# Optimization experiments

Measured on AMD Instinct MI355X. Metric: run time of the kernel, lower is better.

## Reference

```python
import jax, jax.numpy as jnp
import numpy as np
from functools import partial

SOM_SHAPE = (100, 100)
INPUT_SIZE = 256
BATCH = 1024
INIT_LR = 0.5
INIT_RADIUS = max(SOM_SHAPE) / 2.0  # 50.0


def setup_inputs() -> dict:
    key = jax.random.key(0)
    k1, k2 = jax.random.split(key)
    x = jax.random.normal(k1, (BATCH, INPUT_SIZE), dtype=jnp.float32)
    weights = jax.random.normal(k2, (*SOM_SHAPE, INPUT_SIZE), dtype=jnp.float32) * 0.1
    return {"x": x, "weights": weights, "epoch": 10, "total_epochs": 100}


def reference(x, weights, epoch, total_epochs):
    H, W = SOM_SHAPE
    decay = 1.0 - epoch / total_epochs
    lr = jnp.float32(INIT_LR * decay)
    radius = jnp.float32(INIT_RADIUS * decay)

    # --- get_bmu: squared euclidean distances x (B,D) vs weights (H*W,D) ---
    wf = weights.reshape(-1, INPUT_SIZE)                       # (HW, D)
    d2 = (jnp.sum(x * x, axis=1, keepdims=True)                # (B, 1)
          - 2.0 * (x @ wf.T)                                   # (B, HW)
          + jnp.sum(wf * wf, axis=1))                          # (HW,)
    bmu_idx = jnp.argmin(d2, axis=1)                           # (B,)
    by = (bmu_idx // W).astype(jnp.float32)                    # (B,)
    bx = (bmu_idx % W).astype(jnp.float32)

    # --- get_neighborhood: gaussian over grid distance to BMU ---
    yy = jnp.arange(H, dtype=jnp.float32)[:, None]             # (H, 1)
    xx = jnp.arange(W, dtype=jnp.float32)[None, :]             # (1, W)
    grid_d2 = ((by[:, None, None] - yy) ** 2
               + (bx[:, None, None] - xx) ** 2)                # (B, H, W)
    neigh = jnp.exp(-grid_d2 / (2.0 * radius ** 2))            # (B, H, W)

    # --- update_weights: sequential per-sample EMA update (recurrence) ---
    def step(w, inp):
        xi, ni = inp  # (D,), (H, W)
        w = w + lr * ni[..., None] * (xi[None, None, :] - w)
        return w, None

    new_weights, _ = jax.lax.scan(step, weights, (x, neigh))
    return new_weights
```

## Files before the change

kernel.cpp:

```cpp
#include <hip/hip_runtime.h>
#include <hip/hip_fp16.h>

typedef unsigned long long ull;
typedef unsigned short ushort_t;
typedef unsigned int u32;
typedef short bf16x8 __attribute__((ext_vector_type(8)));
typedef _Float16 f16x8 __attribute__((ext_vector_type(8)));
typedef float f32x4 __attribute__((ext_vector_type(4)));

#define NC 10000
#define D_ 256
#define B_ 1024
#define W_ 100
#define LD 10240
#define FIXMARGIN 0.06f
#define SHORTCAP 128

__device__ __forceinline__ void gl_lds16(const void* g, void* l) {
    __builtin_amdgcn_global_load_lds(
        (const __attribute__((address_space(1))) u32*)g,
        (__attribute__((address_space(3))) u32*)l,
        16, 0, 0);
}

__device__ __forceinline__ int xcd_swz(int orig, int nwg) {
    int q = nwg >> 3, r = nwg & 7;
    int xcd = orig & 7, off = orig >> 3;
    return (xcd < r ? xcd * (q + 1) : r * (q + 1) + (xcd - r) * q) + off;
}

__device__ __forceinline__ unsigned fkey(float f) {
    unsigned u = __float_as_uint(f);
    return (u & 0x80000000u) ? ~u : (u | 0x80000000u);
}
__device__ __forceinline__ float unfkey(unsigned k) {
    unsigned u = (k & 0x80000000u) ? (k ^ 0x80000000u) : ~k;
    return __uint_as_float(u);
}

__device__ __forceinline__ ushort_t f2bf(float f) {
    unsigned u = __float_as_uint(f);
    unsigned r = (u + 0x7fffu + ((u >> 16) & 1u)) >> 16;
    return (ushort_t)r;
}

__device__ __forceinline__ void decay_params(const int* ep, const int* tp, float& lr, float& inv2r2) {
    double decay = 1.0 - (double)(*ep) / (double)(*tp);
    lr = (float)(0.5 * decay);
    float radius = (float)(50.0 * decay);
    inv2r2 = 1.0f / (2.0f * radius * radius);
}

__global__ void k_init(ull* pk1, float* wnorm) {
    int i = blockIdx.x * 256 + threadIdx.x;
    if (i < B_) pk1[i] = ~0ull;
    else if (i < B_ + 128) wnorm[NC + (i - B_)] = __builtin_inff();
}

__global__ __launch_bounds__(256) void k_split_w(const float* __restrict__ w, __half* __restrict__ wh,
                                                 float* __restrict__ wnorm) {
    int cell = blockIdx.x * 4 + (threadIdx.x >> 6);
    int lane = threadIdx.x & 63;
    float4 v = *reinterpret_cast<const float4*>(&w[(size_t)cell * D_ + lane * 4]);
    float s = v.x * v.x + v.y * v.y + v.z * v.z + v.w * v.w;
    __half hb[4];
    float e[4] = {v.x, v.y, v.z, v.w};
    #pragma unroll
    for (int i = 0; i < 4; ++i) hb[i] = __float2half(e[i]);
    *reinterpret_cast<uint2*>(&wh[(size_t)cell * D_ + lane * 4]) = *reinterpret_cast<uint2*>(hb);
    #pragma unroll
    for (int off = 32; off; off >>= 1) s += __shfl_xor(s, off);
    if (lane == 0) wnorm[cell] = s;
}

__global__ __launch_bounds__(256) void k_prep_x(const float* __restrict__ x, __half* __restrict__ xh,
                                                ushort_t* __restrict__ xhT) {
    __shared__ ushort_t tile[64][65];
    int b0 = blockIdx.x * 64, d0 = blockIdx.y * 64;
    int tid = threadIdx.x;
    #pragma unroll
    for (int r = 0; r < 16; ++r) {
        int idx = r * 256 + tid;
        int i = idx >> 6, j = idx & 63;
        float v = x[(size_t)(b0 + i) * D_ + d0 + j];
        xh[(size_t)(b0 + i) * D_ + d0 + j] = __float2half(v);
        tile[j][i] = f2bf(v);
    }
    __syncthreads();
    #pragma unroll
    for (int r = 0; r < 2; ++r) {
        int f = r * 256 + tid;
        int row = f >> 3, u = f & 7;
        ushort_t v[8];
        #pragma unroll
        for (int e = 0; e < 8; ++e) v[e] = tile[row][u * 8 + e];
        *reinterpret_cast<uint4*>(&xhT[(size_t)(d0 + row) * B_ + b0 + u * 8]) =
            *reinterpret_cast<uint4*>(v);
    }
}

__global__ __launch_bounds__(512) void k_scores_mfma(const __half* __restrict__ wh, const __half* __restrict__ xh,
                                                     const float* __restrict__ wnorm, __half* __restrict__ h,
                                                     ull* __restrict__ pk1) {
    __shared__ __align__(16) __half As[128 * 64];
    __shared__ __align__(16) __half Bs[128 * 64];
    const int tid = threadIdx.x;
    int orig = blockIdx.y * gridDim.x + blockIdx.x;
    int wgid = xcd_swz(orig, 8 * 79);
    const int b0 = (wgid & 7) * 128;
    const int c0 = (wgid >> 3) * 128;
    const int wid = tid >> 6, lane = tid & 63;
    const int wc = wid >> 2;
    const int wb = wid & 3;
    const int g4 = lane >> 4, l16 = lane & 15;

    f32x4 acc[4][2] = {};

    for (int k0 = 0; k0 < D_; k0 += 64) {
        if (k0) __syncthreads();
        #pragma unroll
        for (int r = 0; r < 2; ++r) {
            int f = tid + r * 512;
            int row = f >> 3, u = f & 7;
            int ug = (u ^ (row & 7)) * 8;
            int cc = c0 + row; if (cc > NC - 1) cc = NC - 1;
            gl_lds16(&wh[(size_t)cc * D_ + k0 + ug], &As[(f & ~63) * 8]);
            gl_lds16(&xh[(size_t)(b0 + row) * D_ + k0 + ug], &Bs[(f & ~63) * 8]);
        }
        __syncthreads();
        #pragma unroll
        for (int kh = 0; kh < 2; ++kh) {
            int ubase = kh * 4 + g4;
            f16x8 bfr[2];
            #pragma unroll
            for (int fn = 0; fn < 2; ++fn) {
                int rowb = wb * 32 + fn * 16 + l16;
                bfr[fn] = *reinterpret_cast<const f16x8*>(&Bs[rowb * 64 + ((ubase ^ (rowb & 7)) * 8)]);
            }
            #pragma unroll
            for (int fm = 0; fm < 4; ++fm) {
                int rowa = wc * 64 + fm * 16 + l16;
                f16x8 af = *reinterpret_cast<const f16x8*>(&As[rowa * 64 + ((ubase ^ (rowa & 7)) * 8)]);
                #pragma unroll
                for (int fn = 0; fn < 2; ++fn)
                    acc[fm][fn] = __builtin_amdgcn_mfma_f32_16x16x32_f16(af, bfr[fn], acc[fm][fn], 0, 0, 0);
            }
        }
    }

    #pragma unroll
    for (int fm = 0; fm < 4; ++fm) {
        int cb = c0 + wc * 64 + fm * 16 + g4 * 4;
        #pragma unroll
        for (int fn = 0; fn < 2; ++fn) {
            int b = b0 + wb * 32 + fn * 16 + l16;
            __half hv[4];
            #pragma unroll
            for (int r = 0; r < 4; ++r) hv[r] = __float2half(acc[fm][fn][r]);
            *reinterpret_cast<uint2*>(&h[(size_t)b * LD + cb]) = *reinterpret_cast<uint2*>(hv);
        }
    }

    ull best[2] = {~0ull, ~0ull};
    #pragma unroll
    for (int fm = 0; fm < 4; ++fm) {
        int cb = c0 + wc * 64 + fm * 16 + g4 * 4;
        float4 wn4 = *reinterpret_cast<const float4*>(&wnorm[cb]);
        float wna[4] = {wn4.x, wn4.y, wn4.z, wn4.w};
        #pragma unroll
        for (int fn = 0; fn < 2; ++fn)
            #pragma unroll
            for (int r = 0; r < 4; ++r) {
                float s = wna[r] - 2.0f * acc[fm][fn][r];
                ull p = ((ull)fkey(s) << 32) | (unsigned)(cb + r);
                if (p < best[fn]) best[fn] = p;
            }
    }
    #pragma unroll
    for (int fn = 0; fn < 2; ++fn) {
        ull o = __shfl_xor(best[fn], 16); best[fn] = o < best[fn] ? o : best[fn];
        o = __shfl_xor(best[fn], 32);     best[fn] = o < best[fn] ? o : best[fn];
    }
    if (g4 == 0) {
        atomicMin(&pk1[b0 + wb * 32 + l16], best[0]);
        atomicMin(&pk1[b0 + wb * 32 + 16 + l16], best[1]);
    }
}

__global__ __launch_bounds__(256) void k_fix(const __half* __restrict__ h, const float* __restrict__ wnorm,
                                             const float* __restrict__ x, const float* __restrict__ w,
                                             const ull* __restrict__ pk1, int2* __restrict__ bxy) {
    __shared__ int cnt;
    __shared__ int cand[SHORTCAP];
    __shared__ ull sbest[4];
    int b = blockIdx.x, tid = threadIdx.x;
    if (tid == 0) cnt = 0;
    __syncthreads();
    float thr = unfkey((unsigned)(pk1[b] >> 32)) + FIXMARGIN;
    for (int ch = 0; ch < 10; ++ch) {
        int c = ch * 1024 + tid * 4;
        if (c < NC) {
            __half hv[4];
            *reinterpret_cast<uint2*>(hv) = *reinterpret_cast<const uint2*>(&h[(size_t)b * LD + c]);
            float4 wn = *reinterpret_cast<const float4*>(&wnorm[c]);
            float we[4] = {wn.x, wn.y, wn.z, wn.w};
            #pragma unroll
            for (int e = 0; e < 4; ++e) {
                float s = we[e] - 2.0f * (float)hv[e];
                if (s <= thr) {
                    int p = atomicAdd(&cnt, 1);
                    if (p < SHORTCAP) cand[p] = c + e;
                }
            }
        }
    }
    __syncthreads();
    int n = cnt;
    int wid = tid >> 6, lane = tid & 63;
    float4 xv = *reinterpret_cast<const float4*>(&x[(size_t)b * D_ + lane * 4]);
    ull best = ~0ull;
    if (n <= SHORTCAP) {
        for (int i = wid; i < n; i += 4) {
            int c = cand[i];
            float4 wv = *reinterpret_cast<const float4*>(&w[(size_t)c * D_ + lane * 4]);
            float p = wv.x * (wv.x - 2.0f * xv.x) + wv.y * (wv.y - 2.0f * xv.y)
                    + wv.z * (wv.z - 2.0f * xv.z) + wv.w * (wv.w - 2.0f * xv.w);
            #pragma unroll
            for (int off = 32; off; off >>= 1) p += __shfl_xor(p, off);
            if (lane == 0) {
                ull pk = ((ull)fkey(p) << 32) | (unsigned)c;
                best = pk < best ? pk : best;
            }
        }
    } else {
        for (int c = wid; c < NC; c += 4) {
            float4 wv = *reinterpret_cast<const float4*>(&w[(size_t)c * D_ + lane * 4]);
            float p = wv.x * (wv.x - 2.0f * xv.x) + wv.y * (wv.y - 2.0f * xv.y)
                    + wv.z * (wv.z - 2.0f * xv.z) + wv.w * (wv.w - 2.0f * xv.w);
            #pragma unroll
            for (int off = 32; off; off >>= 1) p += __shfl_xor(p, off);
            if (lane == 0) {
                ull pk = ((ull)fkey(p) << 32) | (unsigned)c;
                best = pk < best ? pk : best;
            }
        }
    }
    if (lane == 0) sbest[wid] = best;
    __syncthreads();
    if (tid == 0) {
        ull bb = sbest[0];
        #pragma unroll
        for (int k = 1; k < 4; ++k) bb = sbest[k] < bb ? sbest[k] : bb;
        int c = (int)(unsigned)(bb & 0xffffffffull);
        bxy[b] = make_int2(c / W_, c % W_);
    }
}

__global__ __launch_bounds__(256) void k_scan(const int2* __restrict__ bxy, const int* __restrict__ ep,
                                              const int* __restrict__ tp, ushort_t* __restrict__ coefT,
                                              float* __restrict__ T) {
    __shared__ float E[W_];
    float lr, inv2r2;
    decay_params(ep, tp, lr, inv2r2);
    if (threadIdx.x < W_) {
        float d = (float)threadIdx.x;
        E[threadIdx.x] = __expf(-d * d * inv2r2);
    }
    __syncthreads();

    int g = blockIdx.x * 256 + threadIdx.x;
    int c = g >> 3, t = g & 7;
    if (c >= NC) return;
    int cy = c / W_, cx = c % W_;
    int base = t * 128;

    float P = 1.0f;
    for (int i = base; i < base + 128; ++i) {
        int2 p = bxy[i];
        int dy = abs(p.x - cy), dx = abs(p.y - cx);
        float a = lr * E[dy] * E[dx];
        P *= (1.0f - a);
    }
    int gbase = (threadIdx.x & 63) & ~7;
    float M = 1.0f;
    #pragma unroll
    for (int k = 1; k < 8; ++k) {
        float pk = __shfl(P, gbase + k, 64);
        if (k > t) M *= pk;
    }
    if (t == 0) T[c] = M * P;

    float s = M;
    for (int seg = 15; seg >= 0; --seg) {
        ushort_t buf[8];
        #pragma unroll
        for (int e = 7; e >= 0; --e) {
            int i = base + seg * 8 + e;
            int2 p = bxy[i];
            int dy = abs(p.x - cy), dx = abs(p.y - cx);
            float a = lr * E[dy] * E[dx];
            buf[e] = f2bf(a * s);
            s *= (1.0f - a);
        }
        *reinterpret_cast<uint4*>(&coefT[(size_t)c * B_ + base + seg * 8]) =
            *reinterpret_cast<uint4*>(buf);
    }
}

__global__ __launch_bounds__(256) void k_update(const ushort_t* __restrict__ coefT, const ushort_t* __restrict__ xhT,
                                                const float* __restrict__ T, const float* __restrict__ w0,
                                                float* __restrict__ out) {
    __shared__ __align__(16) ushort_t As[64 * 64];
    __shared__ __align__(16) ushort_t Bs[64 * 64];
    const int tid = threadIdx.x;
    int orig = blockIdx.y * gridDim.x + blockIdx.x;
    int wgid = xcd_swz(orig, 4 * 157);
    const int d0 = (wgid & 3) * 64;
    const int c0 = (wgid >> 2) * 64;
    const int wid = tid >> 6, lane = tid & 63;
    const int wc = wid >> 1, wd = wid & 1;
    const int g4 = lane >> 4, l16 = lane & 15;

    f32x4 acc[2][2] = {};

    for (int k0 = 0; k0 < B_; k0 += 64) {
        if (k0) __syncthreads();
        #pragma unroll
        for (int r = 0; r < 2; ++r) {
            int f = tid + r * 256;
            int row = f >> 3, u = f & 7;
            int ug = (u ^ (row & 7)) * 8;
            int cc = c0 + row; if (cc > NC - 1) cc = NC - 1;
            gl_lds16(&coefT[(size_t)cc * B_ + k0 + ug], &As[(f & ~63) * 8]);
            gl_lds16(&xhT[(size_t)(d0 + row) * B_ + k0 + ug], &Bs[(f & ~63) * 8]);
        }
        __syncthreads();
        #pragma unroll
        for (int kh = 0; kh < 2; ++kh) {
            bf16x8 af[2], bfr[2];
            int ubase = kh * 4 + g4;
            #pragma unroll
            for (int fm = 0; fm < 2; ++fm) {
                int rowa = wc * 32 + fm * 16 + l16;
                af[fm] = *reinterpret_cast<const bf16x8*>(&As[rowa * 64 + ((ubase ^ (rowa & 7)) * 8)]);
                int rowb = wd * 32 + fm * 16 + l16;
                bfr[fm] = *reinterpret_cast<const bf16x8*>(&Bs[rowb * 64 + ((ubase ^ (rowb & 7)) * 8)]);
            }
            #pragma unroll
            for (int fm = 0; fm < 2; ++fm)
                #pragma unroll
                for (int fn = 0; fn < 2; ++fn)
                    acc[fm][fn] = __builtin_amdgcn_mfma_f32_16x16x32_bf16(af[fm], bfr[fn], acc[fm][fn], 0, 0, 0);
        }
    }

    #pragma unroll
    for (int fm = 0; fm < 2; ++fm) {
        #pragma unroll
        for (int r = 0; r < 4; ++r) {
            int c = c0 + wc * 32 + fm * 16 + g4 * 4 + r;
            if (c < NC) {
                float t = T[c];
                #pragma unroll
                for (int fn = 0; fn < 2; ++fn) {
                    int d = d0 + wd * 32 + fn * 16 + l16;
                    out[(size_t)c * D_ + d] = fmaf(t, w0[(size_t)c * D_ + d], acc[fm][fn][r]);
                }
            }
        }
    }
}

__global__ void k_initfix(ull* packed_fix) {
    int i = blockIdx.x * 256 + threadIdx.x;
    if (i < B_) packed_fix[i] = ~0ull;
}
__global__ __launch_bounds__(256) void k_exact_bmu(const float* __restrict__ x, const float* __restrict__ w,
                                                   ull* __restrict__ packed_fix) {
    int b = blockIdx.x;
    int wid = threadIdx.x >> 6, lane = threadIdx.x & 63;
    float4 xv = *reinterpret_cast<const float4*>(&x[(size_t)b * D_ + lane * 4]);
    ull best = ~0ull;
    for (int c = wid; c < NC; c += 4) {
        float4 wv = *reinterpret_cast<const float4*>(&w[(size_t)c * D_ + lane * 4]);
        float p = wv.x * (wv.x - 2.0f * xv.x) + wv.y * (wv.y - 2.0f * xv.y)
                + wv.z * (wv.z - 2.0f * xv.z) + wv.w * (wv.w - 2.0f * xv.w);
        #pragma unroll
        for (int off = 32; off; off >>= 1) p += __shfl_xor(p, off);
        if (lane == 0) {
            ull pk = ((ull)fkey(p) << 32) | (unsigned)c;
            best = pk < best ? pk : best;
        }
    }
    if (lane == 0) atomicMin(&packed_fix[b], best);
}
__global__ void k_decode_force(const ull* __restrict__ packed_fix, float2* __restrict__ xy) {
    int i = blockIdx.x * 256 + threadIdx.x;
    if (i < B_) {
        int c = (int)(unsigned)(packed_fix[i] & 0xffffffffull);
        xy[i] = make_float2((float)(c / W_), (float)(c % W_));
    }
}
__global__ __launch_bounds__(256) void k_update_fallback(const float* __restrict__ x, const float* __restrict__ w0,
                                                         const float2* __restrict__ xy, const int* ep, const int* tp,
                                                         float* __restrict__ out) {
    int c = blockIdx.x;
    int d = threadIdx.x;
    float cyf = (float)(c / W_), cxf = (float)(c % W_);
    float lr, inv2r2;
    decay_params(ep, tp, lr, inv2r2);
    float acc = w0[(size_t)c * D_ + d];
    for (int i = 0; i < B_; ++i) {
        float2 p = xy[i];
        float dy = p.x - cyf, dx = p.y - cxf;
        float a = lr * __expf(-(dy * dy + dx * dx) * inv2r2);
        acc = fmaf(a, x[(size_t)i * D_ + d] - acc, acc);
    }
    out[(size_t)c * D_ + d] = acc;
}

extern "C" void kernel_launch(void* const* d_in, const int* in_sizes, int n_in,
                              void* d_out, int out_size, void* d_ws, size_t ws_size,
                              hipStream_t stream) {
    const float* x = (const float*)d_in[0];
    const float* w = (const float*)d_in[1];
    const int* ep = (const int*)d_in[2];
    const int* tp = (const int*)d_in[3];
    float* out = (float*)d_out;

    char* ws = (char*)d_ws;
    ull* pk1        = (ull*)ws;
    int2* bxy       = (int2*)(ws + 16384);
    float2* xyf     = (float2*)(ws + 16384);
    float* T        = (float*)(ws + 24576);
    float* wnorm    = (float*)(ws + 65536);
    ushort_t* xhT   = (ushort_t*)(ws + 131072);
    __half* xh      = (__half*)(ws + 655360);
    __half* wh      = (__half*)(ws + 1179648);
    ushort_t* coefT = (ushort_t*)(ws + 6553600);
    __half* h       = (__half*)(ws + 27262976);
    size_t required = 27262976 + (size_t)B_ * LD * 2;

    if (ws_size >= required) {
        k_init<<<5, 256, 0, stream>>>(pk1, wnorm);
        k_split_w<<<NC / 4, 256, 0, stream>>>(w, wh, wnorm);
        k_prep_x<<<dim3(B_ / 64, D_ / 64), 256, 0, stream>>>(x, xh, xhT);
        k_scores_mfma<<<dim3(B_ / 128, (NC + 127) / 128), 512, 0, stream>>>(wh, xh, wnorm, h, pk1);
        k_fix<<<B_, 256, 0, stream>>>(h, wnorm, x, w, pk1, bxy);
        k_scan<<<(NC * 8 + 255) / 256, 256, 0, stream>>>(bxy, ep, tp, coefT, T);
        k_update<<<dim3(D_ / 64, (NC + 63) / 64), 256, 0, stream>>>(coefT, xhT, T, w, out);
    } else {
        k_initfix<<<4, 256, 0, stream>>>(pk1);
        k_exact_bmu<<<B_, 256, 0, stream>>>(x, w, pk1);
        k_decode_force<<<4, 256, 0, stream>>>(pk1, xyf);
        k_update_fallback<<<NC, 256, 0, stream>>>(x, w, xyf, ep, tp, out);
    }
}
```

Baseline: 92.22 us.

## Replace fp16 score matrix with per-tile top-2 candidates and double-buffer GEMM staging

```diff
diff --git a/kernel.cpp b/kernel.cpp
--- a/kernel.cpp
+++ b/kernel.cpp
@@ -12,9 +12,9 @@
 #define D_ 256
 #define B_ 1024
 #define W_ 100
-#define LD 10240
-#define FIXMARGIN 0.06f
-#define SHORTCAP 128
+#define NT 79
+#define PKS 160
+#define TAU 0.10f
 
 __device__ __forceinline__ void gl_lds16(const void* g, void* l) {
     __builtin_amdgcn_global_load_lds(
@@ -51,64 +51,68 @@
     inv2r2 = 1.0f / (2.0f * radius * radius);
 }
 
-__global__ void k_init(ull* pk1, float* wnorm) {
-    int i = blockIdx.x * 256 + threadIdx.x;
-    if (i < B_) pk1[i] = ~0ull;
-    else if (i < B_ + 128) wnorm[NC + (i - B_)] = __builtin_inff();
-}
-
-__global__ __launch_bounds__(256) void k_split_w(const float* __restrict__ w, __half* __restrict__ wh,
-                                                 float* __restrict__ wnorm) {
-    int cell = blockIdx.x * 4 + (threadIdx.x >> 6);
-    int lane = threadIdx.x & 63;
-    float4 v = *reinterpret_cast<const float4*>(&w[(size_t)cell * D_ + lane * 4]);
-    float s = v.x * v.x + v.y * v.y + v.z * v.z + v.w * v.w;
-    __half hb[4];
-    float e[4] = {v.x, v.y, v.z, v.w};
-    #pragma unroll
-    for (int i = 0; i < 4; ++i) hb[i] = __float2half(e[i]);
-    *reinterpret_cast<uint2*>(&wh[(size_t)cell * D_ + lane * 4]) = *reinterpret_cast<uint2*>(hb);
-    #pragma unroll
-    for (int off = 32; off; off >>= 1) s += __shfl_xor(s, off);
-    if (lane == 0) wnorm[cell] = s;
-}
-
-__global__ __launch_bounds__(256) void k_prep_x(const float* __restrict__ x, __half* __restrict__ xh,
-                                                ushort_t* __restrict__ xhT) {
-    __shared__ ushort_t tile[64][65];
-    int b0 = blockIdx.x * 64, d0 = blockIdx.y * 64;
+__device__ __forceinline__ void merge2(ull& a1, ull& a2, ull c1, ull c2) {
+    ull m1 = a1 < c1 ? a1 : c1;
+    ull hi = a1 < c1 ? c1 : a1;
+    ull lo2 = a2 < c2 ? a2 : c2;
+    a2 = hi < lo2 ? hi : lo2;
+    a1 = m1;
+}
+
+__global__ __launch_bounds__(256) void k_prep(const float* __restrict__ w, const float* __restrict__ x,
+                                              __half* __restrict__ wh, float* __restrict__ wnorm,
+                                              __half* __restrict__ xh, ushort_t* __restrict__ xhT) {
+    int bid = blockIdx.x;
     int tid = threadIdx.x;
-    #pragma unroll
-    for (int r = 0; r < 16; ++r) {
-        int idx = r * 256 + tid;
-        int i = idx >> 6, j = idx & 63;
-        float v = x[(size_t)(b0 + i) * D_ + d0 + j];
-        xh[(size_t)(b0 + i) * D_ + d0 + j] = __float2half(v);
-        tile[j][i] = f2bf(v);
-    }
-    __syncthreads();
-    #pragma unroll
-    for (int r = 0; r < 2; ++r) {
-        int f = r * 256 + tid;
-        int row = f >> 3, u = f & 7;
-        ushort_t v[8];
-        #pragma unroll
-        for (int e = 0; e < 8; ++e) v[e] = tile[row][u * 8 + e];
-        *reinterpret_cast<uint4*>(&xhT[(size_t)(d0 + row) * B_ + b0 + u * 8]) =
-            *reinterpret_cast<uint4*>(v);
+    if (bid < NC / 4) {
+        int cell = bid * 4 + (tid >> 6);
+        int lane = tid & 63;
+        float4 v = *reinterpret_cast<const float4*>(&w[(size_t)cell * D_ + lane * 4]);
+        float s = v.x * v.x + v.y * v.y + v.z * v.z + v.w * v.w;
+        __half hb[4];
+        float e[4] = {v.x, v.y, v.z, v.w};
+        #pragma unroll
+        for (int i = 0; i < 4; ++i) hb[i] = __float2half(e[i]);
+        *reinterpret_cast<uint2*>(&wh[(size_t)cell * D_ + lane * 4]) = *reinterpret_cast<uint2*>(hb);
+        #pragma unroll
+        for (int off = 32; off; off >>= 1) s += __shfl_xor(s, off);
+        if (lane == 0) wnorm[cell] = s;
+    } else {
+        __shared__ ushort_t tile[64][65];
+        int idx = bid - NC / 4;
+        int b0 = (idx & 15) * 64, d0 = (idx >> 4) * 64;
+        #pragma unroll
+        for (int r = 0; r < 16; ++r) {
+            int f = r * 256 + tid;
+            int i = f >> 6, j = f & 63;
+            float v = x[(size_t)(b0 + i) * D_ + d0 + j];
+            xh[(size_t)(b0 + i) * D_ + d0 + j] = __float2half(v);
+            tile[j][i] = f2bf(v);
+        }
+        __syncthreads();
+        #pragma unroll
+        for (int r = 0; r < 2; ++r) {
+            int f = r * 256 + tid;
+            int row = f >> 3, u = f & 7;
+            ushort_t v[8];
+            #pragma unroll
+            for (int e = 0; e < 8; ++e) v[e] = tile[row][u * 8 + e];
+            *reinterpret_cast<uint4*>(&xhT[(size_t)(d0 + row) * B_ + b0 + u * 8]) =
+                *reinterpret_cast<uint4*>(v);
+        }
     }
 }
 
 __global__ __launch_bounds__(512) void k_scores_mfma(const __half* __restrict__ wh, const __half* __restrict__ xh,
-                                                     const float* __restrict__ wnorm, __half* __restrict__ h,
-                                                     ull* __restrict__ pk1) {
-    __shared__ __align__(16) __half As[128 * 64];
-    __shared__ __align__(16) __half Bs[128 * 64];
+                                                     const float* __restrict__ wnorm, ull* __restrict__ pkt) {
+    __shared__ __align__(16) __half As[2][128 * 64];
+    __shared__ __align__(16) __half Bs[2][128 * 64];
     const int tid = threadIdx.x;
     int orig = blockIdx.y * gridDim.x + blockIdx.x;
-    int wgid = xcd_swz(orig, 8 * 79);
+    int wgid = xcd_swz(orig, 8 * NT);
     const int b0 = (wgid & 7) * 128;
     const int c0 = (wgid >> 3) * 128;
+    const int tile = wgid >> 3;
     const int wid = tid >> 6, lane = tid & 63;
     const int wc = wid >> 2;
     const int wb = wid & 3;
@@ -116,18 +120,23 @@
 
     f32x4 acc[4][2] = {};
 
-    for (int k0 = 0; k0 < D_; k0 += 64) {
-        if (k0) __syncthreads();
+    auto STAGE = [&](int buf, int k0) {
         #pragma unroll
         for (int r = 0; r < 2; ++r) {
             int f = tid + r * 512;
             int row = f >> 3, u = f & 7;
             int ug = (u ^ (row & 7)) * 8;
             int cc = c0 + row; if (cc > NC - 1) cc = NC - 1;
-            gl_lds16(&wh[(size_t)cc * D_ + k0 + ug], &As[(f & ~63) * 8]);
-            gl_lds16(&xh[(size_t)(b0 + row) * D_ + k0 + ug], &Bs[(f & ~63) * 8]);
-        }
-        __syncthreads();
+            gl_lds16(&wh[(size_t)cc * D_ + k0 + ug], &As[buf][(f & ~63) * 8]);
+            gl_lds16(&xh[(size_t)(b0 + row) * D_ + k0 + ug], &Bs[buf][(f & ~63) * 8]);
+        }
+    };
+
+    STAGE(0, 0);
+    __syncthreads();
+    for (int kt = 0; kt < 4; ++kt) {
+        int cur = kt & 1;
+        if (kt < 3) STAGE(cur ^ 1, (kt + 1) * 64);
         #pragma unroll
         for (int kh = 0; kh < 2; ++kh) {
             int ubase = kh * 4 + g4;
@@ -135,33 +144,21 @@
             #pragma unroll
             for (int fn = 0; fn < 2; ++fn) {
                 int rowb = wb * 32 + fn * 16 + l16;
-                bfr[fn] = *reinterpret_cast<const f16x8*>(&Bs[rowb * 64 + ((ubase ^ (rowb & 7)) * 8)]);
+                bfr[fn] = *reinterpret_cast<const f16x8*>(&Bs[cur][rowb * 64 + ((ubase ^ (rowb & 7)) * 8)]);
             }
             #pragma unroll
             for (int fm = 0; fm < 4; ++fm) {
                 int rowa = wc * 64 + fm * 16 + l16;
-                f16x8 af = *reinterpret_cast<const f16x8*>(&As[rowa * 64 + ((ubase ^ (rowa & 7)) * 8)]);
+                f16x8 af = *reinterpret_cast<const f16x8*>(&As[cur][rowa * 64 + ((ubase ^ (rowa & 7)) * 8)]);
                 #pragma unroll
                 for (int fn = 0; fn < 2; ++fn)
                     acc[fm][fn] = __builtin_amdgcn_mfma_f32_16x16x32_f16(af, bfr[fn], acc[fm][fn], 0, 0, 0);
             }
         }
-    }
-
-    #pragma unroll
-    for (int fm = 0; fm < 4; ++fm) {
-        int cb = c0 + wc * 64 + fm * 16 + g4 * 4;
-        #pragma unroll
-        for (int fn = 0; fn < 2; ++fn) {
-            int b = b0 + wb * 32 + fn * 16 + l16;
-            __half hv[4];
-            #pragma unroll
-            for (int r = 0; r < 4; ++r) hv[r] = __float2half(acc[fm][fn][r]);
-            *reinterpret_cast<uint2*>(&h[(size_t)b * LD + cb]) = *reinterpret_cast<uint2*>(hv);
-        }
-    }
-
-    ull best[2] = {~0ull, ~0ull};
+        __syncthreads();
+    }
+
+    ull m1[2] = {~0ull, ~0ull}, m2[2] = {~0ull, ~0ull};
     #pragma unroll
     for (int fm = 0; fm < 4; ++fm) {
         int cb = c0 + wc * 64 + fm * 16 + g4 * 4;
@@ -172,86 +169,109 @@
             #pragma unroll
             for (int r = 0; r < 4; ++r) {
                 float s = wna[r] - 2.0f * acc[fm][fn][r];
-                ull p = ((ull)fkey(s) << 32) | (unsigned)(cb + r);
-                if (p < best[fn]) best[fn] = p;
+                ull p = (cb + r < NC) ? (((ull)fkey(s) << 32) | (unsigned)(cb + r)) : ~0ull;
+                merge2(m1[fn], m2[fn], p, ~0ull);
             }
     }
     #pragma unroll
     for (int fn = 0; fn < 2; ++fn) {
-        ull o = __shfl_xor(best[fn], 16); best[fn] = o < best[fn] ? o : best[fn];
-        o = __shfl_xor(best[fn], 32);     best[fn] = o < best[fn] ? o : best[fn];
-    }
+        #pragma unroll
+        for (int off = 16; off <= 32; off <<= 1) {
+            ull o1 = __shfl_xor(m1[fn], off), o2 = __shfl_xor(m2[fn], off);
+            merge2(m1[fn], m2[fn], o1, o2);
+        }
+    }
+    ull* sm1 = (ull*)&As[0][0];
+    ull* sm2 = sm1 + 256;
     if (g4 == 0) {
-        atomicMin(&pk1[b0 + wb * 32 + l16], best[0]);
-        atomicMin(&pk1[b0 + wb * 32 + 16 + l16], best[1]);
-    }
-}
-
-__global__ __launch_bounds__(256) void k_fix(const __half* __restrict__ h, const float* __restrict__ wnorm,
-                                             const float* __restrict__ x, const float* __restrict__ w,
-                                             const ull* __restrict__ pk1, int2* __restrict__ bxy) {
-    __shared__ int cnt;
-    __shared__ int cand[SHORTCAP];
-    __shared__ ull sbest[4];
-    int b = blockIdx.x, tid = threadIdx.x;
-    if (tid == 0) cnt = 0;
-    __syncthreads();
-    float thr = unfkey((unsigned)(pk1[b] >> 32)) + FIXMARGIN;
-    for (int ch = 0; ch < 10; ++ch) {
-        int c = ch * 1024 + tid * 4;
+        #pragma unroll
+        for (int fn = 0; fn < 2; ++fn) {
+            int bl = wb * 32 + fn * 16 + l16;
+            sm1[wc * 128 + bl] = m1[fn];
+            sm2[wc * 128 + bl] = m2[fn];
+        }
+    }
+    __syncthreads();
+    if (tid < 128) {
+        ull a1 = sm1[tid], a2 = sm2[tid];
+        merge2(a1, a2, sm1[128 + tid], sm2[128 + tid]);
+        size_t base = (size_t)(b0 + tid) * PKS + tile * 2;
+        pkt[base] = a1;
+        pkt[base + 1] = a2;
+    }
+}
+
+__global__ __launch_bounds__(128) void k_bmu(const ull* __restrict__ pkt, const float* __restrict__ x,
+                                             const float* __restrict__ w, int2* __restrict__ bxy) {
+    __shared__ ull s1[2], s2[2];
+    __shared__ int candList[NT];
+    __shared__ int candCnt;
+    int b = blockIdx.x;
+    int tid = threadIdx.x, lane = tid & 63, wv = tid >> 6;
+
+    ull a1 = ~0ull, a2 = ~0ull;
+    if (tid < NT) {
+        a1 = pkt[(size_t)b * PKS + tid * 2];
+        a2 = pkt[(size_t)b * PKS + tid * 2 + 1];
+    }
+    #pragma unroll
+    for (int off = 1; off <= 32; off <<= 1) {
+        ull o1 = __shfl_xor(a1, off), o2 = __shfl_xor(a2, off);
+        merge2(a1, a2, o1, o2);
+    }
+    if (lane == 0) { s1[wv] = a1; s2[wv] = a2; }
+    __syncthreads();
+    a1 = s1[0]; a2 = s2[0];
+    merge2(a1, a2, s1[1], s2[1]);
+    float f1 = unfkey((unsigned)(a1 >> 32));
+    float f2 = unfkey((unsigned)(a2 >> 32));
+    if (f2 - f1 >= TAU) {
+        if (tid == 0) {
+            int c = (int)(unsigned)(a1 & 0xffffffffull);
+            bxy[b] = make_int2(c / W_, c % W_);
+        }
+        return;
+    }
+    if (tid == 0) candCnt = 0;
+    __syncthreads();
+    if (tid < NT) {
+        ull mt = pkt[(size_t)b * PKS + tid * 2];
+        if (unfkey((unsigned)(mt >> 32)) <= f1 + TAU) {
+            int p = atomicAdd(&candCnt, 1);
+            candList[p] = tid;
+        }
+    }
+    __syncthreads();
+    int n = candCnt;
+    ull best = ~0ull;
+    const float* xr = &x[(size_t)b * D_];
+    for (int ci = 0; ci < n; ++ci) {
+        int t = candList[ci];
+        int c = t * 128 + tid;
         if (c < NC) {
-            __half hv[4];
-            *reinterpret_cast<uint2*>(hv) = *reinterpret_cast<const uint2*>(&h[(size_t)b * LD + c]);
-            float4 wn = *reinterpret_cast<const float4*>(&wnorm[c]);
-            float we[4] = {wn.x, wn.y, wn.z, wn.w};
-            #pragma unroll
-            for (int e = 0; e < 4; ++e) {
-                float s = we[e] - 2.0f * (float)hv[e];
-                if (s <= thr) {
-                    int p = atomicAdd(&cnt, 1);
-                    if (p < SHORTCAP) cand[p] = c + e;
-                }
-            }
-        }
-    }
-    __syncthreads();
-    int n = cnt;
-    int wid = tid >> 6, lane = tid & 63;
-    float4 xv = *reinterpret_cast<const float4*>(&x[(size_t)b * D_ + lane * 4]);
-    ull best = ~0ull;
-    if (n <= SHORTCAP) {
-        for (int i = wid; i < n; i += 4) {
-            int c = cand[i];
-            float4 wv = *reinterpret_cast<const float4*>(&w[(size_t)c * D_ + lane * 4]);
-            float p = wv.x * (wv.x - 2.0f * xv.x) + wv.y * (wv.y - 2.0f * xv.y)
-                    + wv.z * (wv.z - 2.0f * xv.z) + wv.w * (wv.w - 2.0f * xv.w);
-            #pragma unroll
-            for (int off = 32; off; off >>= 1) p += __shfl_xor(p, off);
-            if (lane == 0) {
-                ull pk = ((ull)fkey(p) << 32) | (unsigned)c;
-                best = pk < best ? pk : best;
-            }
-        }
-    } else {
-        for (int c = wid; c < NC; c += 4) {
-            float4 wv = *reinterpret_cast<const float4*>(&w[(size_t)c * D_ + lane * 4]);
-            float p = wv.x * (wv.x - 2.0f * xv.x) + wv.y * (wv.y - 2.0f * xv.y)
-                    + wv.z * (wv.z - 2.0f * xv.z) + wv.w * (wv.w - 2.0f * xv.w);
-            #pragma unroll
-            for (int off = 32; off; off >>= 1) p += __shfl_xor(p, off);
-            if (lane == 0) {
-                ull pk = ((ull)fkey(p) << 32) | (unsigned)c;
-                best = pk < best ? pk : best;
-            }
-        }
-    }
-    if (lane == 0) sbest[wid] = best;
+            const float* wr = &w[(size_t)c * D_];
+            float p = 0.f;
+            #pragma unroll
+            for (int d = 0; d < D_; d += 4) {
+                float4 wv4 = *reinterpret_cast<const float4*>(&wr[d]);
+                float4 xv4 = *reinterpret_cast<const float4*>(&xr[d]);
+                p += wv4.x * (wv4.x - 2.0f * xv4.x) + wv4.y * (wv4.y - 2.0f * xv4.y)
+                   + wv4.z * (wv4.z - 2.0f * xv4.z) + wv4.w * (wv4.w - 2.0f * xv4.w);
+            }
+            ull pk = ((ull)fkey(p) << 32) | (unsigned)c;
+            best = pk < best ? pk : best;
+        }
+    }
+    #pragma unroll
+    for (int off = 1; off <= 32; off <<= 1) {
+        ull o = __shfl_xor(best, off);
+        best = o < best ? o : best;
+    }
+    if (lane == 0) s1[wv] = best;
     __syncthreads();
     if (tid == 0) {
-        ull bb = sbest[0];
-        #pragma unroll
-        for (int k = 1; k < 4; ++k) bb = sbest[k] < bb ? sbest[k] : bb;
-        int c = (int)(unsigned)(bb & 0xffffffffull);
+        best = s1[0] < s1[1] ? s1[0] : s1[1];
+        int c = (int)(unsigned)(best & 0xffffffffull);
         bxy[b] = make_int2(c / W_, c % W_);
     }
 }
@@ -310,8 +330,8 @@
 __global__ __launch_bounds__(256) void k_update(const ushort_t* __restrict__ coefT, const ushort_t* __restrict__ xhT,
                                                 const float* __restrict__ T, const float* __restrict__ w0,
                                                 float* __restrict__ out) {
-    __shared__ __align__(16) ushort_t As[64 * 64];
-    __shared__ __align__(16) ushort_t Bs[64 * 64];
+    __shared__ __align__(16) ushort_t As[2][64 * 64];
+    __shared__ __align__(16) ushort_t Bs[2][64 * 64];
     const int tid = threadIdx.x;
     int orig = blockIdx.y * gridDim.x + blockIdx.x;
     int wgid = xcd_swz(orig, 4 * 157);
@@ -323,18 +343,23 @@
 
     f32x4 acc[2][2] = {};
 
-    for (int k0 = 0; k0 < B_; k0 += 64) {
-        if (k0) __syncthreads();
+    auto STAGE = [&](int buf, int k0) {
         #pragma unroll
         for (int r = 0; r < 2; ++r) {
             int f = tid + r * 256;
             int row = f >> 3, u = f & 7;
             int ug = (u ^ (row & 7)) * 8;
             int cc = c0 + row; if (cc > NC - 1) cc = NC - 1;
-            gl_lds16(&coefT[(size_t)cc * B_ + k0 + ug], &As[(f & ~63) * 8]);
-            gl_lds16(&xhT[(size_t)(d0 + row) * B_ + k0 + ug], &Bs[(f & ~63) * 8]);
-        }
-        __syncthreads();
+            gl_lds16(&coefT[(size_t)cc * B_ + k0 + ug], &As[buf][(f & ~63) * 8]);
+            gl_lds16(&xhT[(size_t)(d0 + row) * B_ + k0 + ug], &Bs[buf][(f & ~63) * 8]);
+        }
+    };
+
+    STAGE(0, 0);
+    __syncthreads();
+    for (int kt = 0; kt < 16; ++kt) {
+        int cur = kt & 1;
+        if (kt < 15) STAGE(cur ^ 1, (kt + 1) * 64);
         #pragma unroll
         for (int kh = 0; kh < 2; ++kh) {
             bf16x8 af[2], bfr[2];
@@ -342,9 +367,9 @@
             #pragma unroll
             for (int fm = 0; fm < 2; ++fm) {
                 int rowa = wc * 32 + fm * 16 + l16;
-                af[fm] = *reinterpret_cast<const bf16x8*>(&As[rowa * 64 + ((ubase ^ (rowa & 7)) * 8)]);
+                af[fm] = *reinterpret_cast<const bf16x8*>(&As[cur][rowa * 64 + ((ubase ^ (rowa & 7)) * 8)]);
                 int rowb = wd * 32 + fm * 16 + l16;
-                bfr[fm] = *reinterpret_cast<const bf16x8*>(&Bs[rowb * 64 + ((ubase ^ (rowb & 7)) * 8)]);
+                bfr[fm] = *reinterpret_cast<const bf16x8*>(&Bs[cur][rowb * 64 + ((ubase ^ (rowb & 7)) * 8)]);
             }
             #pragma unroll
             for (int fm = 0; fm < 2; ++fm)
@@ -352,6 +377,7 @@
                 for (int fn = 0; fn < 2; ++fn)
                     acc[fm][fn] = __builtin_amdgcn_mfma_f32_16x16x32_bf16(af[fm], bfr[fn], acc[fm][fn], 0, 0, 0);
         }
+        __syncthreads();
     }
 
     #pragma unroll
@@ -429,7 +455,7 @@
     float* out = (float*)d_out;
 
     char* ws = (char*)d_ws;
-    ull* pk1        = (ull*)ws;
+    ull* packed_fix = (ull*)(ws + 8192);
     int2* bxy       = (int2*)(ws + 16384);
     float2* xyf     = (float2*)(ws + 16384);
     float* T        = (float*)(ws + 24576);
@@ -438,21 +464,19 @@
     __half* xh      = (__half*)(ws + 655360);
     __half* wh      = (__half*)(ws + 1179648);
     ushort_t* coefT = (ushort_t*)(ws + 6553600);
-    __half* h       = (__half*)(ws + 27262976);
-    size_t required = 27262976 + (size_t)B_ * LD * 2;
+    ull* pkt        = (ull*)(ws + 27262976);
+    size_t required = 27262976 + (size_t)B_ * PKS * 8;
 
     if (ws_size >= required) {
-        k_init<<<5, 256, 0, stream>>>(pk1, wnorm);
-        k_split_w<<<NC / 4, 256, 0, stream>>>(w, wh, wnorm);
-        k_prep_x<<<dim3(B_ / 64, D_ / 64), 256, 0, stream>>>(x, xh, xhT);
-        k_scores_mfma<<<dim3(B_ / 128, (NC + 127) / 128), 512, 0, stream>>>(wh, xh, wnorm, h, pk1);
-        k_fix<<<B_, 256, 0, stream>>>(h, wnorm, x, w, pk1, bxy);
+        k_prep<<<NC / 4 + 64, 256, 0, stream>>>(w, x, wh, wnorm, xh, xhT);
+        k_scores_mfma<<<dim3(8, NT), 512, 0, stream>>>(wh, xh, wnorm, pkt);
+        k_bmu<<<B_, 128, 0, stream>>>(pkt, x, w, bxy);
         k_scan<<<(NC * 8 + 255) / 256, 256, 0, stream>>>(bxy, ep, tp, coefT, T);
-        k_update<<<dim3(D_ / 64, (NC + 63) / 64), 256, 0, stream>>>(coefT, xhT, T, w, out);
+        k_update<<<dim3(4, 157), 256, 0, stream>>>(coefT, xhT, T, w, out);
     } else {
-        k_initfix<<<4, 256, 0, stream>>>(pk1);
-        k_exact_bmu<<<B_, 256, 0, stream>>>(x, w, pk1);
-        k_decode_force<<<4, 256, 0, stream>>>(pk1, xyf);
+        k_initfix<<<4, 256, 0, stream>>>(packed_fix);
+        k_exact_bmu<<<B_, 256, 0, stream>>>(x, w, packed_fix);
+        k_decode_force<<<4, 256, 0, stream>>>(packed_fix, xyf);
         k_update_fallback<<<NC, 256, 0, stream>>>(x, w, xyf, ep, tp, out);
     }
 }
```

Result: slower. 117.4 us (+27.3%).
